# Kernel optimization log

Measured on AMD Instinct MI355X. Metric: run time of the kernel, lower is better.

The kernel has to match this reference:

```python
import jax, jax.numpy as jnp
import numpy as np

B, OBS, D_MODEL, D_STATE, D_CONV, EXPAND, ACT = 2048, 512, 1024, 16, 4, 2, 18
D_INNER = EXPAND * D_MODEL            # 2048
DT_RANK = (D_MODEL + 15) // 16        # 64

def setup_inputs() -> dict:
    key = jax.random.key(0)
    ks = jax.random.split(key, 20)
    s = 0.02
    return {
        "obs": jax.random.normal(ks[0], (B, OBS), jnp.float32),
        "conv_state": jax.random.normal(ks[1], (B, D_INNER, D_CONV), jnp.float32),
        "ssm_state": jax.random.normal(ks[2], (B, D_INNER, D_STATE), jnp.float32),
        # obs -> d_model projection
        "in_proj_w": jax.random.normal(ks[3], (D_MODEL, OBS), jnp.float32) * s,
        "in_proj_b": jnp.zeros((D_MODEL,), jnp.float32),
        # Mamba in_proj (no bias): d_model -> 2*d_inner (x and z)
        "mamba_in_w": jax.random.normal(ks[4], (2 * D_INNER, D_MODEL), jnp.float32) * s,
        # depthwise causal conv
        "conv_w": jax.random.normal(ks[5], (D_INNER, D_CONV), jnp.float32) * s,
        "conv_b": jnp.zeros((D_INNER,), jnp.float32),
        # x_proj (no bias): d_inner -> dt_rank + 2*d_state
        "x_proj_w": jax.random.normal(ks[6], (DT_RANK + 2 * D_STATE, D_INNER), jnp.float32) * s,
        # dt_proj: dt_rank -> d_inner
        "dt_w": jax.random.normal(ks[7], (D_INNER, DT_RANK), jnp.float32) * s,
        "dt_b": jax.random.normal(ks[8], (D_INNER,), jnp.float32) * s,
        # S4D-style A init: A_log = log(A), A in [1, d_state]
        "A_log": jnp.log(jnp.broadcast_to(jnp.arange(1, D_STATE + 1, dtype=jnp.float32), (D_INNER, D_STATE)) + 0.0),
        "D": jnp.ones((D_INNER,), jnp.float32),
        # out_proj (no bias): d_inner -> d_model
        "out_proj_w": jax.random.normal(ks[9], (D_MODEL, D_INNER), jnp.float32) * s,
        # actor / critic heads
        "pol_w": jax.random.normal(ks[10], (ACT, D_MODEL), jnp.float32) * s,
        "pol_b": jnp.zeros((ACT,), jnp.float32),
        "val_w": jax.random.normal(ks[11], (1, D_MODEL), jnp.float32) * s,
        "val_b": jnp.zeros((1,), jnp.float32),
    }

def _silu(x):
    return x * jax.nn.sigmoid(x)

def reference(obs, conv_state, ssm_state, in_proj_w, in_proj_b, mamba_in_w,
              conv_w, conv_b, x_proj_w, dt_w, dt_b, A_log, D, out_proj_w,
              pol_w, pol_b, val_w, val_b):
    # obs projection: [B, d_model]
    h = obs @ in_proj_w.T + in_proj_b
    # Mamba step (single timestep)
    xz = h @ mamba_in_w.T                        # [B, 2*d_inner]
    x, z = xz[:, :D_INNER], xz[:, D_INNER:]
    # causal depthwise conv via shifted conv_state buffer
    conv_state_new = jnp.concatenate([conv_state[:, :, 1:], x[:, :, None]], axis=-1)  # [B, d_inner, d_conv]
    x = _silu(jnp.sum(conv_state_new * conv_w[None], axis=-1) + conv_b)               # [B, d_inner]
    # input-dependent dt, B, C
    x_db = x @ x_proj_w.T                        # [B, dt_rank + 2*d_state]
    dt = x_db[:, :DT_RANK]
    Bmat = x_db[:, DT_RANK:DT_RANK + D_STATE]    # [B, d_state]
    Cmat = x_db[:, DT_RANK + D_STATE:]           # [B, d_state]
    dt = jax.nn.softplus(dt @ dt_w.T + dt_b)     # [B, d_inner]
    A = -jnp.exp(A_log)                          # [d_inner, d_state]
    dA = jnp.exp(dt[:, :, None] * A[None])       # [B, d_inner, d_state]
    dB = dt[:, :, None] * Bmat[:, None, :]       # [B, d_inner, d_state]
    ssm_state_new = ssm_state * dA + x[:, :, None] * dB
    y = jnp.einsum('bdn,bn->bd', ssm_state_new, Cmat) + D * x
    y = y * _silu(z)
    out = y @ out_proj_w.T                       # [B, d_model]
    logits = out @ pol_w.T + pol_b               # [B, action_dim]
    value = out @ val_w.T + val_b                # [B, 1]
    return logits, value, conv_state_new, ssm_state_new
```

## Files before the change

### kernel.cpp

```cpp
#include <hip/hip_runtime.h>
#include <hip/hip_bf16.h>
#include <math.h>


#define BATCH 2048
#define OBSD 512
#define DMODEL 1024
#define DINNER 2048
#define DSTATE 16
#define DTRANK 64
#define NACT 18

typedef __attribute__((ext_vector_type(8))) short shortx8;
typedef __attribute__((ext_vector_type(4))) float floatx4;

__device__ inline float sig_(float x) { return 1.f / (1.f + __expf(-x)); }

__device__ inline unsigned short bfc(float x) {
    __hip_bfloat16 h = __float2bfloat16(x);
    return *(unsigned short*)&h;
}

__device__ inline void store_bf4(unsigned short* dst, float4 v) {
    ushort4 u;
    u.x = bfc(v.x); u.y = bfc(v.y); u.z = bfc(v.z); u.w = bfc(v.w);
    *(ushort4*)dst = u;
}

__global__ __launch_bounds__(256) void convert_kernel(
    const float* __restrict__ obs, const float* __restrict__ w1,
    const float* __restrict__ w2, const float* __restrict__ w3,
    const float* __restrict__ Alog,
    unsigned short* __restrict__ obs_bf, unsigned short* __restrict__ w1_bf,
    unsigned short* __restrict__ w2_bf, unsigned short* __restrict__ w3_bf,
    float* __restrict__ A_neg)
{
    int g = blockIdx.x * 256 + threadIdx.x;
    if (g < 262144) {
        store_bf4(obs_bf + g * 4, ((const float4*)obs)[g]);
    } else if (g < 393216) {
        int t = g - 262144;
        store_bf4(w1_bf + t * 4, ((const float4*)w1)[t]);
    } else if (g < 1441792) {
        int t = g - 393216;
        store_bf4(w2_bf + t * 4, ((const float4*)w2)[t]);
    } else if (g < 1507328) {
        int t = g - 1441792;
        int e = t * 4;
        int n = e >> 11;
        int k = e & 2047;
        float4 v = {0.f, 0.f, 0.f, 0.f};
        if (n < 96) v = *(const float4*)(w3 + n * 2048 + k);
        store_bf4(w3_bf + e, v);
    } else {
        int t = g - 1507328;
        float4 v = ((const float4*)Alog)[t];
        float4 o = {-__expf(v.x), -__expf(v.y), -__expf(v.z), -__expf(v.w)};
        ((float4*)A_neg)[t] = o;
    }
}

template <int BF16OUT, int BIAS, int SPLITK>
__global__ __launch_bounds__(256) void gemm_bt(
    const short* __restrict__ A, const short* __restrict__ Bm,
    void* __restrict__ Cout, const float* __restrict__ bias,
    int M, int N, int K, int ksplit_len)
{
    __shared__ short As[128 * 32];
    __shared__ short Bs[128 * 32];

    const int tid  = threadIdx.x;
    const int wave = tid >> 6;
    const int lane = tid & 63;
    const int quad = lane >> 4;
    const int l16  = lane & 15;
    const int wm   = (wave & 1) << 6;
    const int wn   = (wave >> 1) << 6;
    const int bm   = blockIdx.x;
    const int bn   = blockIdx.y;

    int kbeg = 0, kend = K;
    if (SPLITK) { kbeg = blockIdx.z * ksplit_len; kend = kbeg + ksplit_len; }

    floatx4 acc[4][4] = {};

    const int v0 = tid * 8;
    const int r0 = v0 >> 5, c0 = v0 & 31;
    const int v1 = (256 + tid) * 8;
    const int r1 = v1 >> 5, c1 = v1 & 31;

    const short* Abase = A + (size_t)bm * 128 * K;
    const short* Bbase = Bm + (size_t)bn * 128 * K;

    for (int k0 = kbeg; k0 < kend; k0 += 32) {
        __syncthreads();
        __builtin_amdgcn_global_load_lds(
            (const __attribute__((address_space(1))) unsigned int*)(Abase + (size_t)r0 * K + k0 + c0),
            (__attribute__((address_space(3))) unsigned int*)(As + wave * 512), 16, 0, 0);
        __builtin_amdgcn_global_load_lds(
            (const __attribute__((address_space(1))) unsigned int*)(Abase + (size_t)r1 * K + k0 + c1),
            (__attribute__((address_space(3))) unsigned int*)(As + 2048 + wave * 512), 16, 0, 0);
        __builtin_amdgcn_global_load_lds(
            (const __attribute__((address_space(1))) unsigned int*)(Bbase + (size_t)r0 * K + k0 + c0),
            (__attribute__((address_space(3))) unsigned int*)(Bs + wave * 512), 16, 0, 0);
        __builtin_amdgcn_global_load_lds(
            (const __attribute__((address_space(1))) unsigned int*)(Bbase + (size_t)r1 * K + k0 + c1),
            (__attribute__((address_space(3))) unsigned int*)(Bs + 2048 + wave * 512), 16, 0, 0);
        __syncthreads();

        shortx8 af[4], bfv[4];
#pragma unroll
        for (int i = 0; i < 4; ++i)
            af[i] = *(const shortx8*)(As + (wm + i * 16 + l16) * 32 + quad * 8);
#pragma unroll
        for (int j = 0; j < 4; ++j)
            bfv[j] = *(const shortx8*)(Bs + (wn + j * 16 + l16) * 32 + quad * 8);
#pragma unroll
        for (int i = 0; i < 4; ++i)
#pragma unroll
            for (int j = 0; j < 4; ++j)
                acc[i][j] = __builtin_amdgcn_mfma_f32_16x16x32_bf16(af[i], bfv[j], acc[i][j], 0, 0, 0);
    }

    if (BF16OUT) {
        unsigned short* C = (unsigned short*)Cout;
#pragma unroll
        for (int i = 0; i < 4; ++i) {
            int gm = bm * 128 + wm + i * 16 + quad * 4;
#pragma unroll
            for (int j = 0; j < 4; ++j) {
                int gn = bn * 128 + wn + j * 16 + l16;
                float bv = BIAS ? bias[gn] : 0.f;
#pragma unroll
                for (int r = 0; r < 4; ++r)
                    C[(size_t)(gm + r) * N + gn] = bfc(acc[i][j][r] + bv);
            }
        }
    } else {
        float* C = (float*)Cout;
        if (SPLITK) C += (size_t)blockIdx.z * M * N;
#pragma unroll
        for (int i = 0; i < 4; ++i) {
            int gm = bm * 128 + wm + i * 16 + quad * 4;
#pragma unroll
            for (int j = 0; j < 4; ++j) {
                int gn = bn * 128 + wn + j * 16 + l16;
                float bv = BIAS ? bias[gn] : 0.f;
#pragma unroll
                for (int r = 0; r < 4; ++r)
                    C[(size_t)(gm + r) * N + gn] = acc[i][j][r] + bv;
            }
        }
    }
}

__global__ __launch_bounds__(256) void gemm_g2(
    const short* __restrict__ A, const short* __restrict__ Bm,
    const float* __restrict__ conv_state, const float* __restrict__ conv_w,
    const float* __restrict__ conv_b, float* __restrict__ conv_out,
    float* __restrict__ x_conv, unsigned short* __restrict__ x_conv_bf,
    float* __restrict__ zs, int K)
{
    __shared__ short As[128 * 32];
    __shared__ short Bs[128 * 32];

    const int tid  = threadIdx.x;
    const int wave = tid >> 6;
    const int lane = tid & 63;
    const int quad = lane >> 4;
    const int l16  = lane & 15;
    const int wm   = (wave & 1) << 6;
    const int wn   = (wave >> 1) << 6;
    const int bm   = blockIdx.x;
    const int bn   = blockIdx.y;

    floatx4 acc[4][4] = {};

    const int v0 = tid * 8;
    const int r0 = v0 >> 5, c0 = v0 & 31;
    const int v1 = (256 + tid) * 8;
    const int r1 = v1 >> 5, c1 = v1 & 31;

    const short* Abase = A + (size_t)bm * 128 * K;
    const short* Bbase = Bm + (size_t)bn * 128 * K;

    for (int k0 = 0; k0 < K; k0 += 32) {
        __syncthreads();
        __builtin_amdgcn_global_load_lds(
            (const __attribute__((address_space(1))) unsigned int*)(Abase + (size_t)r0 * K + k0 + c0),
            (__attribute__((address_space(3))) unsigned int*)(As + wave * 512), 16, 0, 0);
        __builtin_amdgcn_global_load_lds(
            (const __attribute__((address_space(1))) unsigned int*)(Abase + (size_t)r1 * K + k0 + c1),
            (__attribute__((address_space(3))) unsigned int*)(As + 2048 + wave * 512), 16, 0, 0);
        __builtin_amdgcn_global_load_lds(
            (const __attribute__((address_space(1))) unsigned int*)(Bbase + (size_t)r0 * K + k0 + c0),
            (__attribute__((address_space(3))) unsigned int*)(Bs + wave * 512), 16, 0, 0);
        __builtin_amdgcn_global_load_lds(
            (const __attribute__((address_space(1))) unsigned int*)(Bbase + (size_t)r1 * K + k0 + c1),
            (__attribute__((address_space(3))) unsigned int*)(Bs + 2048 + wave * 512), 16, 0, 0);
        __syncthreads();

        shortx8 af[4], bfv[4];
#pragma unroll
        for (int i = 0; i < 4; ++i)
            af[i] = *(const shortx8*)(As + (wm + i * 16 + l16) * 32 + quad * 8);
#pragma unroll
        for (int j = 0; j < 4; ++j)
            bfv[j] = *(const shortx8*)(Bs + (wn + j * 16 + l16) * 32 + quad * 8);
#pragma unroll
        for (int i = 0; i < 4; ++i)
#pragma unroll
            for (int j = 0; j < 4; ++j)
                acc[i][j] = __builtin_amdgcn_mfma_f32_16x16x32_bf16(af[i], bfv[j], acc[i][j], 0, 0, 0);
    }

    if (bn < 16) {
#pragma unroll
        for (int j = 0; j < 4; ++j) {
            int d = bn * 128 + wn + j * 16 + l16;
            float4 w4 = *(const float4*)(conv_w + d * 4);
            float cb = conv_b[d];
#pragma unroll
            for (int i = 0; i < 4; ++i) {
                int gm = bm * 128 + wm + i * 16 + quad * 4;
#pragma unroll
                for (int r = 0; r < 4; ++r) {
                    size_t idx = (size_t)(gm + r) * 2048 + d;
                    float xv = acc[i][j][r];
                    float4 cs = *(const float4*)(conv_state + idx * 4);
                    float s = cs.y * w4.x + cs.z * w4.y + cs.w * w4.z + xv * w4.w + cb;
                    float xc = s * sig_(s);
                    float4 outv = {cs.y, cs.z, cs.w, xv};
                    *(float4*)(conv_out + idx * 4) = outv;
                    x_conv[idx] = xc;
                    x_conv_bf[idx] = bfc(xc);
                }
            }
        }
    } else {
#pragma unroll
        for (int j = 0; j < 4; ++j) {
            int d = bn * 128 + wn + j * 16 + l16 - 2048;
#pragma unroll
            for (int i = 0; i < 4; ++i) {
                int gm = bm * 128 + wm + i * 16 + quad * 4;
#pragma unroll
                for (int r = 0; r < 4; ++r) {
                    float zv = acc[i][j][r];
                    zs[(size_t)(gm + r) * 2048 + d] = zv * sig_(zv);
                }
            }
        }
    }
}

__global__ __launch_bounds__(256) void reduce_g3(
    const float* __restrict__ part, float* __restrict__ x_db)
{
    int idx = blockIdx.x * 256 + threadIdx.x;
    int b = idx / 96, n = idx - b * 96;
    float s = 0.f;
#pragma unroll
    for (int z = 0; z < 8; ++z)
        s += part[(size_t)z * BATCH * 128 + b * 128 + n];
    x_db[idx] = s;
}

__global__ __launch_bounds__(256) void dt_kernel(
    const float* __restrict__ x_db, const float* __restrict__ dt_w,
    const float* __restrict__ dt_b, float* __restrict__ dt_full)
{
    __shared__ float dtp[8][64];
    int tid = threadIdx.x;
    int b0 = blockIdx.y * 8;
    {
        int bb = tid >> 5, k = tid & 31;
        dtp[bb][k]      = x_db[(b0 + bb) * 96 + k];
        dtp[bb][k + 32] = x_db[(b0 + bb) * 96 + k + 32];
    }
    __syncthreads();
    int d = blockIdx.x * 256 + tid;
    float acc[8];
    float bv = dt_b[d];
#pragma unroll
    for (int bb = 0; bb < 8; ++bb) acc[bb] = bv;
    const float4* w = (const float4*)(dt_w + d * 64);
#pragma unroll
    for (int k4 = 0; k4 < 16; ++k4) {
        float4 wv = w[k4];
#pragma unroll
        for (int bb = 0; bb < 8; ++bb) {
            acc[bb] += dtp[bb][k4 * 4 + 0] * wv.x + dtp[bb][k4 * 4 + 1] * wv.y +
                       dtp[bb][k4 * 4 + 2] * wv.z + dtp[bb][k4 * 4 + 3] * wv.w;
        }
    }
#pragma unroll
    for (int bb = 0; bb < 8; ++bb) {
        float a = acc[bb];
        float sp = a > 20.f ? a : log1pf(__expf(a));
        dt_full[(size_t)(b0 + bb) * 2048 + d] = sp;
    }
}

__global__ __launch_bounds__(256) void ssm_kernel(
    const float* __restrict__ ssm_state, const float* __restrict__ x_conv,
    const float* __restrict__ dt_full, const float* __restrict__ zs,
    const float* __restrict__ x_db, const float* __restrict__ A_neg,
    const float* __restrict__ Dvec, float* __restrict__ ssm_out,
    unsigned short* __restrict__ y_bf)
{
    __shared__ float BC[32];
    int b = blockIdx.y;
    int tid = threadIdx.x;
    if (tid < 32) BC[tid] = x_db[b * 96 + 64 + tid];
    __syncthreads();
    int q  = tid & 3;
    int d  = blockIdx.x * 64 + (tid >> 2);
    size_t idx = (size_t)b * 2048 + d;
    float x  = x_conv[idx];
    float dt = dt_full[idx];
    float xdt = x * dt;
    float4 s = *(const float4*)(ssm_state + idx * 16 + q * 4);
    float4 a = *(const float4*)(A_neg + d * 16 + q * 4);
    float4 o;
    o.x = s.x * __expf(dt * a.x) + xdt * BC[q * 4 + 0];
    o.y = s.y * __expf(dt * a.y) + xdt * BC[q * 4 + 1];
    o.z = s.z * __expf(dt * a.z) + xdt * BC[q * 4 + 2];
    o.w = s.w * __expf(dt * a.w) + xdt * BC[q * 4 + 3];
    *(float4*)(ssm_out + idx * 16 + q * 4) = o;
    float p = o.x * BC[16 + q * 4 + 0] + o.y * BC[16 + q * 4 + 1] +
              o.z * BC[16 + q * 4 + 2] + o.w * BC[16 + q * 4 + 3];
    p += __shfl_xor(p, 1);
    p += __shfl_xor(p, 2);
    if (q == 0) {
        float y = p + Dvec[d] * x;
        y *= zs[idx];
        y_bf[idx] = bfc(y);
    }
}

__global__ __launch_bounds__(256) void fold_heads(
    const float* __restrict__ opw, const float* __restrict__ pol_w,
    const float* __restrict__ val_w, float* __restrict__ Wc)
{
    __shared__ float hw[1024];
    int j = blockIdx.y;
    const float* src = (j < 18) ? (pol_w + j * 1024) : val_w;
    for (int t = threadIdx.x; t < 1024; t += 256) hw[t] = src[t];
    __syncthreads();
    int d = blockIdx.x * 256 + threadIdx.x;
    float acc = 0.f;
#pragma unroll 8
    for (int m = 0; m < 1024; ++m)
        acc += hw[m] * opw[(size_t)m * 2048 + d];
    Wc[j * 2048 + d] = acc;
}

__global__ __launch_bounds__(256) void heads_kernel(
    const unsigned short* __restrict__ y_bf, const float* __restrict__ Wc,
    const float* __restrict__ pol_b, const float* __restrict__ val_b,
    float* __restrict__ logits, float* __restrict__ value)
{
    __shared__ __align__(16) float row[2048];
    int b = blockIdx.x;
    int tid = threadIdx.x;
    shortx8 v = ((const shortx8*)(y_bf + (size_t)b * 2048))[tid];
#pragma unroll
    for (int e = 0; e < 8; ++e) {
        unsigned int u = ((unsigned int)(unsigned short)v[e]) << 16;
        row[tid * 8 + e] = *(float*)&u;
    }
    __syncthreads();
    int wave = tid >> 6, lane = tid & 63;
    for (int j = wave; j < 19; j += 4) {
        const float4* w = (const float4*)(Wc + j * 2048);
        float p = 0.f;
        for (int k4 = lane; k4 < 512; k4 += 64) {
            float4 wv = w[k4];
            float4 rv = ((const float4*)row)[k4];
            p += rv.x * wv.x + rv.y * wv.y + rv.z * wv.z + rv.w * wv.w;
        }
#pragma unroll
        for (int off = 32; off; off >>= 1) p += __shfl_down(p, off);
        if (lane == 0) {
            if (j < 18) logits[b * NACT + j] = p + pol_b[j];
            else        value[b] = p + val_b[0];
        }
    }
}

extern "C" void kernel_launch(void* const* d_in, const int* in_sizes, int n_in,
                              void* d_out, int out_size, void* d_ws, size_t ws_size,
                              hipStream_t stream)
{
    const float* obs        = (const float*)d_in[0];
    const float* conv_state = (const float*)d_in[1];
    const float* ssm_state  = (const float*)d_in[2];
    const float* in_proj_w  = (const float*)d_in[3];
    const float* in_proj_b  = (const float*)d_in[4];
    const float* mamba_in_w = (const float*)d_in[5];
    const float* conv_w     = (const float*)d_in[6];
    const float* conv_b     = (const float*)d_in[7];
    const float* x_proj_w   = (const float*)d_in[8];
    const float* dt_w       = (const float*)d_in[9];
    const float* dt_b       = (const float*)d_in[10];
    const float* A_log      = (const float*)d_in[11];
    const float* Dvec       = (const float*)d_in[12];
    const float* out_proj_w = (const float*)d_in[13];
    const float* pol_w      = (const float*)d_in[14];
    const float* pol_b      = (const float*)d_in[15];
    const float* val_w      = (const float*)d_in[16];
    const float* val_b      = (const float*)d_in[17];

    char* ws = (char*)d_ws;
    unsigned short* obs_bf    = (unsigned short*)(ws + 0);
    unsigned short* w1_bf     = (unsigned short*)(ws + 2097152);
    unsigned short* w2_bf     = (unsigned short*)(ws + 3145728);
    unsigned short* w3_bf     = (unsigned short*)(ws + 11534336);
    float*          A_neg     = (float*)(ws + 12058624);
    unsigned short* h_bf      = (unsigned short*)(ws + 12189696);
    float*          x_conv    = (float*)(ws + 16384000);
    unsigned short* x_conv_bf = (unsigned short*)(ws + 33161216);
    float*          zs        = (float*)(ws + 41549824);
    float*          g3_part   = (float*)(ws + 58327040);
    float*          x_db      = (float*)(ws + 66715648);
    float*          dt_full   = (float*)(ws + 67502080);
    unsigned short* y_bf      = (unsigned short*)(ws + 84279296);
    float*          Wc        = (float*)(ws + 92667904);
    if (ws_size < 92823552) return;

    float* logits   = (float*)d_out;
    float* value    = logits + (size_t)BATCH * NACT;
    float* conv_out = value + BATCH;
    float* ssm_out  = conv_out + (size_t)BATCH * DINNER * 4;

    convert_kernel<<<5920, 256, 0, stream>>>(obs, in_proj_w, mamba_in_w, x_proj_w,
                                             A_log, obs_bf, w1_bf, w2_bf, w3_bf,
                                             A_neg);

    fold_heads<<<dim3(8, 19), 256, 0, stream>>>(out_proj_w, pol_w, val_w, Wc);

    gemm_bt<1, 1, 0><<<dim3(16, 8), 256, 0, stream>>>(
        (const short*)obs_bf, (const short*)w1_bf, h_bf, in_proj_b, 2048, 1024, 512, 0);

    gemm_g2<<<dim3(16, 32), 256, 0, stream>>>(
        (const short*)h_bf, (const short*)w2_bf, conv_state, conv_w, conv_b,
        conv_out, x_conv, x_conv_bf, zs, 1024);

    gemm_bt<0, 0, 1><<<dim3(16, 1, 8), 256, 0, stream>>>(
        (const short*)x_conv_bf, (const short*)w3_bf, g3_part, nullptr, 2048, 128, 2048, 256);
    reduce_g3<<<768, 256, 0, stream>>>(g3_part, x_db);

    dt_kernel<<<dim3(8, 256), 256, 0, stream>>>(x_db, dt_w, dt_b, dt_full);

    ssm_kernel<<<dim3(32, 2048), 256, 0, stream>>>(ssm_state, x_conv, dt_full, zs,
                                                   x_db, A_neg, Dvec, ssm_out, y_bf);

    heads_kernel<<<2048, 256, 0, stream>>>(y_bf, Wc, pol_b, val_b, logits, value);
}
```

Before: 855.6 us.

## Double-buffer GEMM tiles and fuse split-K reduce, SSM, heads and fold kernels

Several changes at once. The fold_heads work moves into the convert kernel as extra blocks, and the split-K reduction moves into dt_kernel. The SSM update and the policy/value heads become one per-batch-row kernel that keeps y in shared memory instead of writing and re-reading it as bf16. Separately, both GEMM kernels now double-buffer their LDS tiles so the next K-slice loads while the current one computes. The goal is fewer launches and less intermediate global traffic. The costs are larger LDS use per GEMM block and a much smaller SSM grid (2048 blocks, each looping over 32 rows), which may expose memory latency.

```diff
diff --git a/kernel.cpp b/kernel.cpp
--- a/kernel.cpp
+++ b/kernel.cpp
@@ -27,15 +27,33 @@
     *(ushort4*)dst = u;
 }
 
-__global__ __launch_bounds__(256) void convert_kernel(
+__global__ __launch_bounds__(256) void convert_fold_kernel(
     const float* __restrict__ obs, const float* __restrict__ w1,
     const float* __restrict__ w2, const float* __restrict__ w3,
-    const float* __restrict__ Alog,
+    const float* __restrict__ Alog, const float* __restrict__ opw,
+    const float* __restrict__ pol_w, const float* __restrict__ val_w,
     unsigned short* __restrict__ obs_bf, unsigned short* __restrict__ w1_bf,
     unsigned short* __restrict__ w2_bf, unsigned short* __restrict__ w3_bf,
-    float* __restrict__ A_neg)
-{
-    int g = blockIdx.x * 256 + threadIdx.x;
+    float* __restrict__ A_neg, float* __restrict__ Wc)
+{
+    int blk = blockIdx.x;
+    if (blk >= 5920) {
+        __shared__ float hw[1024];
+        int idx = blk - 5920;
+        int j = idx % 19;
+        int dblk = idx / 19;
+        const float* src = (j < 18) ? (pol_w + j * 1024) : val_w;
+        for (int t = threadIdx.x; t < 1024; t += 256) hw[t] = src[t];
+        __syncthreads();
+        int d = dblk * 256 + threadIdx.x;
+        float acc = 0.f;
+#pragma unroll 8
+        for (int m = 0; m < 1024; ++m)
+            acc += hw[m] * opw[(size_t)m * 2048 + d];
+        Wc[j * 2048 + d] = acc;
+        return;
+    }
+    int g = blk * 256 + threadIdx.x;
     if (g < 262144) {
         store_bf4(obs_bf + g * 4, ((const float4*)obs)[g]);
     } else if (g < 393216) {
@@ -60,14 +78,32 @@
     }
 }
 
+__device__ __forceinline__ void stage_tile(
+    const short* Abase, const short* Bbase, short* As, short* Bs,
+    int K, int k0, int wave, int r0, int c0, int r1, int c1)
+{
+    __builtin_amdgcn_global_load_lds(
+        (const __attribute__((address_space(1))) unsigned int*)(Abase + (size_t)r0 * K + k0 + c0),
+        (__attribute__((address_space(3))) unsigned int*)(As + wave * 512), 16, 0, 0);
+    __builtin_amdgcn_global_load_lds(
+        (const __attribute__((address_space(1))) unsigned int*)(Abase + (size_t)r1 * K + k0 + c1),
+        (__attribute__((address_space(3))) unsigned int*)(As + 2048 + wave * 512), 16, 0, 0);
+    __builtin_amdgcn_global_load_lds(
+        (const __attribute__((address_space(1))) unsigned int*)(Bbase + (size_t)r0 * K + k0 + c0),
+        (__attribute__((address_space(3))) unsigned int*)(Bs + wave * 512), 16, 0, 0);
+    __builtin_amdgcn_global_load_lds(
+        (const __attribute__((address_space(1))) unsigned int*)(Bbase + (size_t)r1 * K + k0 + c1),
+        (__attribute__((address_space(3))) unsigned int*)(Bs + 2048 + wave * 512), 16, 0, 0);
+}
+
 template <int BF16OUT, int BIAS, int SPLITK>
 __global__ __launch_bounds__(256) void gemm_bt(
     const short* __restrict__ A, const short* __restrict__ Bm,
     void* __restrict__ Cout, const float* __restrict__ bias,
     int M, int N, int K, int ksplit_len)
 {
-    __shared__ short As[128 * 32];
-    __shared__ short Bs[128 * 32];
+    __shared__ short As[2][128 * 32];
+    __shared__ short Bs[2][128 * 32];
 
     const int tid  = threadIdx.x;
     const int wave = tid >> 6;
@@ -92,34 +128,28 @@
     const short* Abase = A + (size_t)bm * 128 * K;
     const short* Bbase = Bm + (size_t)bn * 128 * K;
 
+    stage_tile(Abase, Bbase, As[0], Bs[0], K, kbeg, wave, r0, c0, r1, c1);
+    __syncthreads();
+
+    int cur = 0;
     for (int k0 = kbeg; k0 < kend; k0 += 32) {
-        __syncthreads();
-        __builtin_amdgcn_global_load_lds(
-            (const __attribute__((address_space(1))) unsigned int*)(Abase + (size_t)r0 * K + k0 + c0),
-            (__attribute__((address_space(3))) unsigned int*)(As + wave * 512), 16, 0, 0);
-        __builtin_amdgcn_global_load_lds(
-            (const __attribute__((address_space(1))) unsigned int*)(Abase + (size_t)r1 * K + k0 + c1),
-            (__attribute__((address_space(3))) unsigned int*)(As + 2048 + wave * 512), 16, 0, 0);
-        __builtin_amdgcn_global_load_lds(
-            (const __attribute__((address_space(1))) unsigned int*)(Bbase + (size_t)r0 * K + k0 + c0),
-            (__attribute__((address_space(3))) unsigned int*)(Bs + wave * 512), 16, 0, 0);
-        __builtin_amdgcn_global_load_lds(
-            (const __attribute__((address_space(1))) unsigned int*)(Bbase + (size_t)r1 * K + k0 + c1),
-            (__attribute__((address_space(3))) unsigned int*)(Bs + 2048 + wave * 512), 16, 0, 0);
-        __syncthreads();
-
+        if (k0 + 32 < kend)
+            stage_tile(Abase, Bbase, As[cur ^ 1], Bs[cur ^ 1], K, k0 + 32,
+                       wave, r0, c0, r1, c1);
         shortx8 af[4], bfv[4];
 #pragma unroll
         for (int i = 0; i < 4; ++i)
-            af[i] = *(const shortx8*)(As + (wm + i * 16 + l16) * 32 + quad * 8);
+            af[i] = *(const shortx8*)(As[cur] + (wm + i * 16 + l16) * 32 + quad * 8);
 #pragma unroll
         for (int j = 0; j < 4; ++j)
-            bfv[j] = *(const shortx8*)(Bs + (wn + j * 16 + l16) * 32 + quad * 8);
+            bfv[j] = *(const shortx8*)(Bs[cur] + (wn + j * 16 + l16) * 32 + quad * 8);
 #pragma unroll
         for (int i = 0; i < 4; ++i)
 #pragma unroll
             for (int j = 0; j < 4; ++j)
                 acc[i][j] = __builtin_amdgcn_mfma_f32_16x16x32_bf16(af[i], bfv[j], acc[i][j], 0, 0, 0);
+        __syncthreads();
+        cur ^= 1;
     }
 
     if (BF16OUT) {
@@ -161,8 +191,8 @@
     float* __restrict__ x_conv, unsigned short* __restrict__ x_conv_bf,
     float* __restrict__ zs, int K)
 {
-    __shared__ short As[128 * 32];
-    __shared__ short Bs[128 * 32];
+    __shared__ short As[2][128 * 32];
+    __shared__ short Bs[2][128 * 32];
 
     const int tid  = threadIdx.x;
     const int wave = tid >> 6;
@@ -184,34 +214,28 @@
     const short* Abase = A + (size_t)bm * 128 * K;
     const short* Bbase = Bm + (size_t)bn * 128 * K;
 
+    stage_tile(Abase, Bbase, As[0], Bs[0], K, 0, wave, r0, c0, r1, c1);
+    __syncthreads();
+
+    int cur = 0;
     for (int k0 = 0; k0 < K; k0 += 32) {
-        __syncthreads();
-        __builtin_amdgcn_global_load_lds(
-            (const __attribute__((address_space(1))) unsigned int*)(Abase + (size_t)r0 * K + k0 + c0),
-            (__attribute__((address_space(3))) unsigned int*)(As + wave * 512), 16, 0, 0);
-        __builtin_amdgcn_global_load_lds(
-            (const __attribute__((address_space(1))) unsigned int*)(Abase + (size_t)r1 * K + k0 + c1),
-            (__attribute__((address_space(3))) unsigned int*)(As + 2048 + wave * 512), 16, 0, 0);
-        __builtin_amdgcn_global_load_lds(
-            (const __attribute__((address_space(1))) unsigned int*)(Bbase + (size_t)r0 * K + k0 + c0),
-            (__attribute__((address_space(3))) unsigned int*)(Bs + wave * 512), 16, 0, 0);
-        __builtin_amdgcn_global_load_lds(
-            (const __attribute__((address_space(1))) unsigned int*)(Bbase + (size_t)r1 * K + k0 + c1),
-            (__attribute__((address_space(3))) unsigned int*)(Bs + 2048 + wave * 512), 16, 0, 0);
-        __syncthreads();
-
+        if (k0 + 32 < K)
+            stage_tile(Abase, Bbase, As[cur ^ 1], Bs[cur ^ 1], K, k0 + 32,
+                       wave, r0, c0, r1, c1);
         shortx8 af[4], bfv[4];
 #pragma unroll
         for (int i = 0; i < 4; ++i)
-            af[i] = *(const shortx8*)(As + (wm + i * 16 + l16) * 32 + quad * 8);
+            af[i] = *(const shortx8*)(As[cur] + (wm + i * 16 + l16) * 32 + quad * 8);
 #pragma unroll
         for (int j = 0; j < 4; ++j)
-            bfv[j] = *(const shortx8*)(Bs + (wn + j * 16 + l16) * 32 + quad * 8);
+            bfv[j] = *(const shortx8*)(Bs[cur] + (wn + j * 16 + l16) * 32 + quad * 8);
 #pragma unroll
         for (int i = 0; i < 4; ++i)
 #pragma unroll
             for (int j = 0; j < 4; ++j)
                 acc[i][j] = __builtin_amdgcn_mfma_f32_16x16x32_bf16(af[i], bfv[j], acc[i][j], 0, 0, 0);
+        __syncthreads();
+        cur ^= 1;
     }
 
     if (bn < 16) {
@@ -254,29 +278,32 @@
     }
 }
 
-__global__ __launch_bounds__(256) void reduce_g3(
-    const float* __restrict__ part, float* __restrict__ x_db)
-{
-    int idx = blockIdx.x * 256 + threadIdx.x;
-    int b = idx / 96, n = idx - b * 96;
-    float s = 0.f;
-#pragma unroll
-    for (int z = 0; z < 8; ++z)
-        s += part[(size_t)z * BATCH * 128 + b * 128 + n];
-    x_db[idx] = s;
-}
-
 __global__ __launch_bounds__(256) void dt_kernel(
-    const float* __restrict__ x_db, const float* __restrict__ dt_w,
-    const float* __restrict__ dt_b, float* __restrict__ dt_full)
+    const float* __restrict__ part, const float* __restrict__ dt_w,
+    const float* __restrict__ dt_b, float* __restrict__ dt_full,
+    float* __restrict__ x_db)
 {
     __shared__ float dtp[8][64];
     int tid = threadIdx.x;
     int b0 = blockIdx.y * 8;
     {
         int bb = tid >> 5, k = tid & 31;
-        dtp[bb][k]      = x_db[(b0 + bb) * 96 + k];
-        dtp[bb][k + 32] = x_db[(b0 + bb) * 96 + k + 32];
+        size_t base = ((size_t)(b0 + bb)) * 128;
+        float s0 = 0.f, s1 = 0.f;
+#pragma unroll
+        for (int z = 0; z < 8; ++z) {
+            s0 += part[(size_t)z * BATCH * 128 + base + k];
+            s1 += part[(size_t)z * BATCH * 128 + base + k + 32];
+        }
+        dtp[bb][k]      = s0;
+        dtp[bb][k + 32] = s1;
+        if (blockIdx.x == 0) {
+            float s2 = 0.f;
+#pragma unroll
+            for (int z = 0; z < 8; ++z)
+                s2 += part[(size_t)z * BATCH * 128 + base + 64 + k];
+            x_db[(b0 + bb) * 96 + 64 + k] = s2;
+        }
     }
     __syncthreads();
     int d = blockIdx.x * 256 + tid;
@@ -302,73 +329,45 @@
     }
 }
 
-__global__ __launch_bounds__(256) void ssm_kernel(
+__global__ __launch_bounds__(256) void ssm_heads_kernel(
     const float* __restrict__ ssm_state, const float* __restrict__ x_conv,
     const float* __restrict__ dt_full, const float* __restrict__ zs,
     const float* __restrict__ x_db, const float* __restrict__ A_neg,
-    const float* __restrict__ Dvec, float* __restrict__ ssm_out,
-    unsigned short* __restrict__ y_bf)
+    const float* __restrict__ Dvec, const float* __restrict__ Wc,
+    const float* __restrict__ pol_b, const float* __restrict__ val_b,
+    float* __restrict__ ssm_out, float* __restrict__ logits,
+    float* __restrict__ value)
 {
     __shared__ float BC[32];
-    int b = blockIdx.y;
+    __shared__ __align__(16) float yrow[2048];
+    int b = blockIdx.x;
     int tid = threadIdx.x;
     if (tid < 32) BC[tid] = x_db[b * 96 + 64 + tid];
     __syncthreads();
-    int q  = tid & 3;
-    int d  = blockIdx.x * 64 + (tid >> 2);
-    size_t idx = (size_t)b * 2048 + d;
-    float x  = x_conv[idx];
-    float dt = dt_full[idx];
-    float xdt = x * dt;
-    float4 s = *(const float4*)(ssm_state + idx * 16 + q * 4);
-    float4 a = *(const float4*)(A_neg + d * 16 + q * 4);
-    float4 o;
-    o.x = s.x * __expf(dt * a.x) + xdt * BC[q * 4 + 0];
-    o.y = s.y * __expf(dt * a.y) + xdt * BC[q * 4 + 1];
-    o.z = s.z * __expf(dt * a.z) + xdt * BC[q * 4 + 2];
-    o.w = s.w * __expf(dt * a.w) + xdt * BC[q * 4 + 3];
-    *(float4*)(ssm_out + idx * 16 + q * 4) = o;
-    float p = o.x * BC[16 + q * 4 + 0] + o.y * BC[16 + q * 4 + 1] +
-              o.z * BC[16 + q * 4 + 2] + o.w * BC[16 + q * 4 + 3];
-    p += __shfl_xor(p, 1);
-    p += __shfl_xor(p, 2);
-    if (q == 0) {
-        float y = p + Dvec[d] * x;
-        y *= zs[idx];
-        y_bf[idx] = bfc(y);
-    }
-}
-
-__global__ __launch_bounds__(256) void fold_heads(
-    const float* __restrict__ opw, const float* __restrict__ pol_w,
-    const float* __restrict__ val_w, float* __restrict__ Wc)
-{
-    __shared__ float hw[1024];
-    int j = blockIdx.y;
-    const float* src = (j < 18) ? (pol_w + j * 1024) : val_w;
-    for (int t = threadIdx.x; t < 1024; t += 256) hw[t] = src[t];
-    __syncthreads();
-    int d = blockIdx.x * 256 + threadIdx.x;
-    float acc = 0.f;
-#pragma unroll 8
-    for (int m = 0; m < 1024; ++m)
-        acc += hw[m] * opw[(size_t)m * 2048 + d];
-    Wc[j * 2048 + d] = acc;
-}
-
-__global__ __launch_bounds__(256) void heads_kernel(
-    const unsigned short* __restrict__ y_bf, const float* __restrict__ Wc,
-    const float* __restrict__ pol_b, const float* __restrict__ val_b,
-    float* __restrict__ logits, float* __restrict__ value)
-{
-    __shared__ __align__(16) float row[2048];
-    int b = blockIdx.x;
-    int tid = threadIdx.x;
-    shortx8 v = ((const shortx8*)(y_bf + (size_t)b * 2048))[tid];
-#pragma unroll
-    for (int e = 0; e < 8; ++e) {
-        unsigned int u = ((unsigned int)(unsigned short)v[e]) << 16;
-        row[tid * 8 + e] = *(float*)&u;
+    int q = tid & 3;
+    int dl = tid >> 2;
+    for (int r = 0; r < 32; ++r) {
+        int d = r * 64 + dl;
+        size_t idx = (size_t)b * 2048 + d;
+        float x  = x_conv[idx];
+        float dt = dt_full[idx];
+        float xdt = x * dt;
+        float4 s = *(const float4*)(ssm_state + idx * 16 + q * 4);
+        float4 a = *(const float4*)(A_neg + (size_t)d * 16 + q * 4);
+        float4 o;
+        o.x = s.x * __expf(dt * a.x) + xdt * BC[q * 4 + 0];
+        o.y = s.y * __expf(dt * a.y) + xdt * BC[q * 4 + 1];
+        o.z = s.z * __expf(dt * a.z) + xdt * BC[q * 4 + 2];
+        o.w = s.w * __expf(dt * a.w) + xdt * BC[q * 4 + 3];
+        *(float4*)(ssm_out + idx * 16 + q * 4) = o;
+        float p = o.x * BC[16 + q * 4 + 0] + o.y * BC[16 + q * 4 + 1] +
+                  o.z * BC[16 + q * 4 + 2] + o.w * BC[16 + q * 4 + 3];
+        p += __shfl_xor(p, 1);
+        p += __shfl_xor(p, 2);
+        if (q == 0) {
+            float y = p + Dvec[d] * x;
+            yrow[d] = y * zs[idx];
+        }
     }
     __syncthreads();
     int wave = tid >> 6, lane = tid & 63;
@@ -377,7 +376,7 @@
         float p = 0.f;
         for (int k4 = lane; k4 < 512; k4 += 64) {
             float4 wv = w[k4];
-            float4 rv = ((const float4*)row)[k4];
+            float4 rv = ((const float4*)yrow)[k4];
             p += rv.x * wv.x + rv.y * wv.y + rv.z * wv.z + rv.w * wv.w;
         }
 #pragma unroll
@@ -425,20 +424,17 @@
     float*          g3_part   = (float*)(ws + 58327040);
     float*          x_db      = (float*)(ws + 66715648);
     float*          dt_full   = (float*)(ws + 67502080);
-    unsigned short* y_bf      = (unsigned short*)(ws + 84279296);
-    float*          Wc        = (float*)(ws + 92667904);
-    if (ws_size < 92823552) return;
+    float*          Wc        = (float*)(ws + 84279296);
+    if (ws_size < 84434944) return;
 
     float* logits   = (float*)d_out;
     float* value    = logits + (size_t)BATCH * NACT;
     float* conv_out = value + BATCH;
     float* ssm_out  = conv_out + (size_t)BATCH * DINNER * 4;
 
-    convert_kernel<<<5920, 256, 0, stream>>>(obs, in_proj_w, mamba_in_w, x_proj_w,
-                                             A_log, obs_bf, w1_bf, w2_bf, w3_bf,
-                                             A_neg);
-
-    fold_heads<<<dim3(8, 19), 256, 0, stream>>>(out_proj_w, pol_w, val_w, Wc);
+    convert_fold_kernel<<<6072, 256, 0, stream>>>(
+        obs, in_proj_w, mamba_in_w, x_proj_w, A_log, out_proj_w, pol_w, val_w,
+        obs_bf, w1_bf, w2_bf, w3_bf, A_neg, Wc);
 
     gemm_bt<1, 1, 0><<<dim3(16, 8), 256, 0, stream>>>(
         (const short*)obs_bf, (const short*)w1_bf, h_bf, in_proj_b, 2048, 1024, 512, 0);
@@ -449,12 +445,10 @@
 
     gemm_bt<0, 0, 1><<<dim3(16, 1, 8), 256, 0, stream>>>(
         (const short*)x_conv_bf, (const short*)w3_bf, g3_part, nullptr, 2048, 128, 2048, 256);
-    reduce_g3<<<768, 256, 0, stream>>>(g3_part, x_db);
-
-    dt_kernel<<<dim3(8, 256), 256, 0, stream>>>(x_db, dt_w, dt_b, dt_full);
-
-    ssm_kernel<<<dim3(32, 2048), 256, 0, stream>>>(ssm_state, x_conv, dt_full, zs,
-                                                   x_db, A_neg, Dvec, ssm_out, y_bf);
-
-    heads_kernel<<<2048, 256, 0, stream>>>(y_bf, Wc, pol_b, val_b, logits, value);
-}
+
+    dt_kernel<<<dim3(8, 256), 256, 0, stream>>>(g3_part, dt_w, dt_b, dt_full, x_db);
+
+    ssm_heads_kernel<<<2048, 256, 0, stream>>>(
+        ssm_state, x_conv, dt_full, zs, x_db, A_neg, Dvec, Wc, pol_b, val_b,
+        ssm_out, logits, value);
+}
```

Result: no change. 859.1 us (+0.4%).
